# Kernel optimization log

Measured on AMD Instinct MI355X. Metric: run time of the kernel, lower is better.

The kernel has to match this reference:

```python
import jax, jax.numpy as jnp
import numpy as np

DIM = 1024
HDS = 16
HEAD_DIM = DIM // HDS
ISC = True


def setup_inputs() -> dict:
    key = jax.random.key(0)
    k = jax.random.split(key, 5)
    x = jax.random.normal(k[0], (4, 2048, DIM), dtype=jnp.float32)
    # Linear(dim, 3*dim): weight [3*dim, dim] (torch layout), bias [3*dim]
    scale = 1.0 / np.sqrt(DIM)
    w_qkv = jax.random.uniform(k[1], (3 * DIM, DIM), jnp.float32, -scale, scale)
    b_qkv = jax.random.uniform(k[2], (3 * DIM,), jnp.float32, -scale, scale)
    w_out = jax.random.uniform(k[3], (DIM, DIM), jnp.float32, -scale, scale)
    b_out = jax.random.uniform(k[4], (DIM,), jnp.float32, -scale, scale)
    return {"x": x, "w_qkv": w_qkv, "b_qkv": b_qkv, "w_out": w_out, "b_out": b_out}


def reference(x, w_qkv, b_qkv, w_out, b_out):
    b, s, dim = x.shape
    # QKV projection: x @ w_qkv.T + b_qkv -> split into q, k, v
    qkv = jnp.einsum('bsd,ed->bse', x, w_qkv) + b_qkv
    q, k, v = jnp.split(qkv, 3, axis=-1)
    # [b, s, dim] -> [b, h, s, hd]
    def to_heads(t):
        return t.reshape(b, s, HDS, HEAD_DIM).transpose(0, 2, 1, 3)
    q, k, v = to_heads(q), to_heads(k), to_heads(v)
    att = jnp.einsum('bhqd,bhkd->bhqk', q, k) * (HEAD_DIM ** -0.5)
    if ISC:
        mask = jnp.triu(jnp.ones((s, s), dtype=bool), k=1)  # True above diagonal
        att = jnp.where(mask[None, None], -jnp.inf, att)
    att = jax.nn.softmax(att, axis=-1)
    # dropout is identity in eval mode
    out = jnp.einsum('bhqk,bhkd->bhqd', att, v)
    out = out.transpose(0, 2, 1, 3).reshape(b, s, dim)
    out = jnp.einsum('bsd,ed->bse', out, w_out) + b_out
    return out
```

## Files before the change

kernel.cpp:

```cpp
#include <hip/hip_runtime.h>
#include <stdint.h>

typedef __bf16 bf16x8 __attribute__((ext_vector_type(8)));
typedef short s16x8 __attribute__((ext_vector_type(8)));
typedef short s16x4 __attribute__((ext_vector_type(4)));
typedef float f32x4 __attribute__((ext_vector_type(4)));
typedef unsigned short u16;

#define K_DIM 1024

static __device__ __forceinline__ u16 f2bf(float f) {
    uint32_t x = __float_as_uint(f);
    x += 0x7fffu + ((x >> 16) & 1u);
    return (u16)(x >> 16);
}

static __device__ __forceinline__ f32x4 mfma16(s16x8 a, s16x8 b, f32x4 c) {
    return __builtin_amdgcn_mfma_f32_16x16x32_bf16(
        __builtin_bit_cast(bf16x8, a), __builtin_bit_cast(bf16x8, b), c, 0, 0, 0);
}

static __device__ __forceinline__ void gload16(const u16* g, u16* l) {
    __builtin_amdgcn_global_load_lds(
        (const __attribute__((address_space(1))) void*)g,
        (__attribute__((address_space(3))) void*)l,
        16, 0, 0);
}

static __device__ __forceinline__ uint32_t cvt_pk_bf16(float lo, float hi) {
    uint32_t r;
    asm("v_cvt_pk_bf16_f32 %0, %1, %2" : "=v"(r) : "v"(lo), "v"(hi));
    return r;
}

static __device__ __forceinline__ float fexp2(float x) {
#if __has_builtin(__builtin_amdgcn_exp2f)
    return __builtin_amdgcn_exp2f(x);
#else
    return __expf(x * 0.69314718056f);
#endif
}

__global__ void cvt_f2bf(const float* __restrict__ in, u16* __restrict__ out, int n4) {
    int stride = gridDim.x * blockDim.x;
    for (int i = blockIdx.x * blockDim.x + threadIdx.x; i < n4; i += stride) {
        float4 f = ((const float4*)in)[i];
        ushort4 o;
        o.x = f2bf(f.x); o.y = f2bf(f.y); o.z = f2bf(f.z); o.w = f2bf(f.w);
        ((ushort4*)out)[i] = o;
    }
}

__global__ __launch_bounds__(256) void gemm_qkv(
    const u16* __restrict__ A, const u16* __restrict__ B,
    const float* __restrict__ bias,
    u16* __restrict__ qo, u16* __restrict__ ko, u16* __restrict__ vto)
{
    __shared__ u16 smem[32768];
    u16* ct = smem;
    const int tid = threadIdx.x;
    const int w = tid >> 6, l = tid & 63;
    const int lr = l & 15, lc = l >> 4;

    const int f = blockIdx.y * 64 + blockIdx.x;
    const int c = f & 7, j = f >> 3;
    const int m0 = (c * 8 + (j & 7)) * 128;
    const int n0 = (j >> 3) * 128;
    const int wm = (w >> 1) * 64, wn = (w & 1) * 64;

    const int srow = w * 8 + (l >> 3);
    const int scol = ((l & 7) ^ (l >> 3)) * 8;
    const u16* gA = A + (size_t)(m0 + srow) * K_DIM + scol;
    const u16* gB = B + (size_t)(n0 + srow) * K_DIM + scol;

    f32x4 acc[4][4] = {};

    auto stage = [&](int k0, int buf) {
        u16* base = smem + buf * 16384;
        #pragma unroll
        for (int g = 0; g < 4; ++g) {
            gload16(gA + (size_t)g * 32 * K_DIM + k0, base + (g * 32 + w * 8) * 64);
            gload16(gB + (size_t)g * 32 * K_DIM + k0, base + 8192 + (g * 32 + w * 8) * 64);
        }
    };

    stage(0, 0);
    int cur = 0;

    for (int k0 = 0; k0 < K_DIM; k0 += 64) {
        __syncthreads();
        if (k0 + 64 < K_DIM) stage(k0 + 64, cur ^ 1);
        const u16* As = smem + cur * 16384;
        const u16* Bs = As + 8192;
        #pragma unroll
        for (int kk = 0; kk < 2; ++kk) {
            s16x8 a[4], b[4];
            #pragma unroll
            for (int i = 0; i < 4; ++i) {
                const int row = wm + i * 16 + lr;
                a[i] = *(const s16x8*)&As[row * 64 + ((kk * 32 + lc * 8) ^ ((row & 7) * 8))];
            }
            #pragma unroll
            for (int jn = 0; jn < 4; ++jn) {
                const int row = wn + jn * 16 + lr;
                b[jn] = *(const s16x8*)&Bs[row * 64 + ((kk * 32 + lc * 8) ^ ((row & 7) * 8))];
            }
            #pragma unroll
            for (int i = 0; i < 4; ++i)
                #pragma unroll
                for (int jn = 0; jn < 4; ++jn)
                    acc[i][jn] = mfma16(a[i], b[jn], acc[i][jn]);
        }
        cur ^= 1;
    }

    const int sec = n0 >> 10;
    const int bb = m0 >> 11, s0 = m0 & 2047;

    if (sec < 2) {
        #pragma unroll
        for (int jn = 0; jn < 4; ++jn) {
            const int n = n0 + wn + jn * 16 + lr;
            const float bv = bias[n];
            const int h = (n & 1023) >> 6, d = n & 63;
            #pragma unroll
            for (int i = 0; i < 4; ++i) {
                #pragma unroll
                for (int r = 0; r < 4; ++r) {
                    const int m = m0 + wm + i * 16 + lc * 4 + r;
                    const int s = m & 2047;
                    float v = acc[i][jn][r] + bv;
                    if (sec == 0)
                        qo[((size_t)((bb * 16 + h) * 2048 + s)) * 64 + d] = f2bf(v * 0.18033688f);
                    else
                        ko[((size_t)((bb * 16 + h) * 2048 + s)) * 64 + d] = f2bf(v);
                }
            }
        }
    } else {
        __syncthreads();
        #pragma unroll
        for (int jj = 0; jj < 4; ++jj) {
            const int nl = (wn >> 6) * 16 + lr;
            const float bv = bias[n0 + wn + jj * 16 + lr];
            #pragma unroll
            for (int i = 0; i < 4; ++i) {
                const int mloc = wm + i * 16 + lc * 4;
                uint2 pk;
                pk.x = cvt_pk_bf16(acc[i][jj][0] + bv, acc[i][jj][1] + bv);
                pk.y = cvt_pk_bf16(acc[i][jj][2] + bv, acc[i][jj][3] + bv);
                *(s16x4*)&ct[nl * 136 + mloc] = __builtin_bit_cast(s16x4, pk);
            }
            __syncthreads();
            #pragma unroll
            for (int rep = 0; rep < 2; ++rep) {
                const int col = tid >> 3;
                const int seg = (tid & 7) + rep * 8;
                const int nn = n0 + (col >> 4) * 64 + jj * 16 + (col & 15);
                const int h = (nn & 1023) >> 6, d = nn & 63;
                const int mo = seg * 8;
                s16x8 v = *(const s16x8*)&ct[col * 136 + mo];
                *(s16x8*)&vto[((size_t)((bb * 16 + h) * 64 + d)) * 2048 + s0 + mo] = v;
            }
            __syncthreads();
        }
    }
}

__global__ __launch_bounds__(256, 2) void attn_fwd(
    const u16* __restrict__ q, const u16* __restrict__ k,
    const u16* __restrict__ vt, u16* __restrict__ ao)
{
    __shared__ u16 kt[2][8 * 512];
    __shared__ u16 vtl[2][8 * 512];
    __shared__ u16 plds[4 * 32 * 72];
    const int w = threadIdx.x >> 6, l = threadIdx.x & 63;
    const int lr = l & 15, lc = l >> 4;
    const int bh = blockIdx.x;
    const int cp = blockIdx.y;
    const u16* qp = q + (size_t)bh * 2048 * 64;
    const u16* kp = k + (size_t)bh * 2048 * 64;
    const u16* vp = vt + (size_t)bh * 64 * 2048;
    u16* pl = &plds[w * 2304];
    const int bb = bh >> 4, h = bh & 15;

    for (int pass = 0; pass < 2; ++pass) {
        const int C = pass ? (15 - cp) : cp;
        const int q0 = C * 128 + w * 32;
        const int nb = 2 * C + 2;
        const int diag = 2 * C + (w >> 1);

        s16x8 aQ[2][2];
        #pragma unroll
        for (int i = 0; i < 2; ++i)
            #pragma unroll
            for (int kk = 0; kk < 2; ++kk)
                aQ[i][kk] = *(const s16x8*)&qp[(q0 + i * 16 + lr) * 64 + kk * 32 + lc * 8];

        f32x4 O[2][4] = {};
        f32x4 lsv[2] = {};

        auto stage = [&](int t, int buf) {
            const int c0 = t * 64;
            if (w < 2) {
                #pragma unroll
                for (int gi = 0; gi < 4; ++gi) {
                    const int g = w * 4 + gi;
                    const int jx = g >> 1, kk = g & 1;
                    gload16(kp + (c0 + jx * 16 + lr) * 64 + kk * 32 + lc * 8,
                            &kt[buf][g * 512]);
                }
            } else {
                #pragma unroll
                for (int gi = 0; gi < 4; ++gi) {
                    const int g = (w - 2) * 4 + gi;
                    const int jd = g >> 1, kk = g & 1;
                    gload16(vp + (jd * 16 + lr) * 2048 + c0 + kk * 32 + lc * 8,
                            &vtl[buf][g * 512]);
                }
            }
        };

        __syncthreads();
        stage(0, 0);
        int cur = 0;

        for (int t = 0; t < nb; ++t) {
            __syncthreads();
            if (t + 1 < nb) stage(t + 1, cur ^ 1);

            if (t <= diag) {
                const int c0 = t * 64;
                f32x4 s[2][4] = {};
                __builtin_amdgcn_s_setprio(1);
                #pragma unroll
                for (int jx = 0; jx < 4; ++jx) {
                    s16x8 k0 = *(const s16x8*)&kt[cur][(jx * 2 + 0) * 512 + l * 8];
                    s16x8 k1 = *(const s16x8*)&kt[cur][(jx * 2 + 1) * 512 + l * 8];
                    s[0][jx] = mfma16(k0, aQ[0][0], s[0][jx]);
                    s[0][jx] = mfma16(k1, aQ[0][1], s[0][jx]);
                    s[1][jx] = mfma16(k0, aQ[1][0], s[1][jx]);
                    s[1][jx] = mfma16(k1, aQ[1][1], s[1][jx]);
                }
                __builtin_amdgcn_s_setprio(0);
                if (t == diag) {
                    #pragma unroll
                    for (int i = 0; i < 2; ++i) {
                        const int qrow = q0 + i * 16 + lr;
                        #pragma unroll
                        for (int jx = 0; jx < 4; ++jx) {
                            const int kvb = c0 + jx * 16 + lc * 4;
                            #pragma unroll
                            for (int r = 0; r < 4; ++r)
                                if (kvb + r > qrow) s[i][jx][r] = -1e30f;
                        }
                    }
                }
                #pragma unroll
                for (int i = 0; i < 2; ++i) {
                    #pragma unroll
                    for (int jx = 0; jx < 4; ++jx)
                        #pragma unroll
                        for (int r = 0; r < 4; ++r)
                            s[i][jx][r] = fexp2(s[i][jx][r]);
                    lsv[i] += (s[i][0] + s[i][1]) + (s[i][2] + s[i][3]);
                    #pragma unroll
                    for (int jx = 0; jx < 4; ++jx) {
                        uint2 pk;
                        pk.x = cvt_pk_bf16(s[i][jx][0], s[i][jx][1]);
                        pk.y = cvt_pk_bf16(s[i][jx][2], s[i][jx][3]);
                        *(s16x4*)&pl[(i * 16 + lr) * 72 + jx * 16 + lc * 4] =
                            __builtin_bit_cast(s16x4, pk);
                    }
                }
                s16x8 aP[2][2];
                #pragma unroll
                for (int i = 0; i < 2; ++i)
                    #pragma unroll
                    for (int kk = 0; kk < 2; ++kk)
                        aP[i][kk] = *(const s16x8*)&pl[(i * 16 + lr) * 72 + kk * 32 + lc * 8];
                __builtin_amdgcn_s_setprio(1);
                #pragma unroll
                for (int jd = 0; jd < 4; ++jd) {
                    s16x8 v0 = *(const s16x8*)&vtl[cur][(jd * 2 + 0) * 512 + l * 8];
                    s16x8 v1 = *(const s16x8*)&vtl[cur][(jd * 2 + 1) * 512 + l * 8];
                    O[0][jd] = mfma16(aP[0][0], v0, O[0][jd]);
                    O[0][jd] = mfma16(aP[0][1], v1, O[0][jd]);
                    O[1][jd] = mfma16(aP[1][0], v0, O[1][jd]);
                    O[1][jd] = mfma16(aP[1][1], v1, O[1][jd]);
                }
                __builtin_amdgcn_s_setprio(0);
            }
            cur ^= 1;
        }

        float lsr[2];
        #pragma unroll
        for (int i = 0; i < 2; ++i) {
            float t2 = (lsv[i][0] + lsv[i][1]) + (lsv[i][2] + lsv[i][3]);
            t2 += __shfl_xor(t2, 16);
            t2 += __shfl_xor(t2, 32);
            lsr[i] = 1.0f / t2;
        }
        float inv[2][4];
        #pragma unroll
        for (int i = 0; i < 2; ++i)
            #pragma unroll
            for (int r = 0; r < 4; ++r)
                inv[i][r] = __shfl(lsr[i], lc * 4 + r);

        #pragma unroll
        for (int i = 0; i < 2; ++i)
            #pragma unroll
            for (int jd = 0; jd < 4; ++jd)
                #pragma unroll
                for (int r = 0; r < 4; ++r) {
                    const int srow = q0 + i * 16 + lc * 4 + r;
                    ao[((size_t)(bb * 2048 + srow)) * 1024 + h * 64 + jd * 16 + lr] =
                        f2bf(O[i][jd][r] * inv[i][r]);
                }
    }
}

__global__ __launch_bounds__(256) void gemm_out(
    const u16* __restrict__ A, const u16* __restrict__ B,
    const float* __restrict__ bias, float* __restrict__ out)
{
    __shared__ u16 smem[32768];
    const int tid = threadIdx.x;
    const int w = tid >> 6, l = tid & 63;
    const int lr = l & 15, lc = l >> 4;

    const int f = blockIdx.y * 64 + blockIdx.x;
    const int c = f & 7, j = f >> 3;
    const int m0 = (c * 8 + (j & 7)) * 128;
    const int n0 = (j >> 3) * 128;
    const int wm = (w >> 1) * 64, wn = (w & 1) * 64;

    const int srow = w * 8 + (l >> 3);
    const int scol = ((l & 7) ^ (l >> 3)) * 8;
    const u16* gA = A + (size_t)(m0 + srow) * K_DIM + scol;
    const u16* gB = B + (size_t)(n0 + srow) * K_DIM + scol;

    f32x4 acc[4][4] = {};

    auto stage = [&](int k0, int buf) {
        u16* base = smem + buf * 16384;
        #pragma unroll
        for (int g = 0; g < 4; ++g) {
            gload16(gA + (size_t)g * 32 * K_DIM + k0, base + (g * 32 + w * 8) * 64);
            gload16(gB + (size_t)g * 32 * K_DIM + k0, base + 8192 + (g * 32 + w * 8) * 64);
        }
    };

    stage(0, 0);
    int cur = 0;

    for (int k0 = 0; k0 < K_DIM; k0 += 64) {
        __syncthreads();
        if (k0 + 64 < K_DIM) stage(k0 + 64, cur ^ 1);
        const u16* As = smem + cur * 16384;
        const u16* Bs = As + 8192;
        #pragma unroll
        for (int kk = 0; kk < 2; ++kk) {
            s16x8 a[4], b[4];
            #pragma unroll
            for (int i = 0; i < 4; ++i) {
                const int row = wm + i * 16 + lr;
                a[i] = *(const s16x8*)&As[row * 64 + ((kk * 32 + lc * 8) ^ ((row & 7) * 8))];
            }
            #pragma unroll
            for (int jn = 0; jn < 4; ++jn) {
                const int row = wn + jn * 16 + lr;
                b[jn] = *(const s16x8*)&Bs[row * 64 + ((kk * 32 + lc * 8) ^ ((row & 7) * 8))];
            }
            #pragma unroll
            for (int i = 0; i < 4; ++i)
                #pragma unroll
                for (int jn = 0; jn < 4; ++jn)
                    acc[i][jn] = mfma16(a[i], b[jn], acc[i][jn]);
        }
        cur ^= 1;
    }

    #pragma unroll
    for (int jn = 0; jn < 4; ++jn) {
        const int n = n0 + wn + jn * 16 + lr;
        const float bv = bias[n];
        #pragma unroll
        for (int i = 0; i < 4; ++i) {
            #pragma unroll
            for (int r = 0; r < 4; ++r) {
                const int m = m0 + wm + i * 16 + lc * 4 + r;
                out[(size_t)m * 1024 + n] = acc[i][jn][r] + bv;
            }
        }
    }
}

extern "C" void kernel_launch(void* const* d_in, const int* in_sizes, int n_in,
                              void* d_out, int out_size, void* d_ws, size_t ws_size,
                              hipStream_t stream) {
    const float* x     = (const float*)d_in[0];
    const float* w_qkv = (const float*)d_in[1];
    const float* b_qkv = (const float*)d_in[2];
    const float* w_out = (const float*)d_in[3];
    const float* b_out = (const float*)d_in[4];
    float* out = (float*)d_out;

    char* ws = (char*)d_ws;
    u16* xb   = (u16*)(ws);
    u16* wqb  = (u16*)(ws + 16777216);
    u16* wob  = (u16*)(ws + 23068672);
    u16* qws  = (u16*)(ws + 25165824);
    u16* kws  = (u16*)(ws + 41943040);
    u16* vtws = (u16*)(ws + 58720256);
    u16* attn = (u16*)(ws + 75497472);

    cvt_f2bf<<<dim3(2048), 256, 0, stream>>>(x,     xb,  8388608 / 4);
    cvt_f2bf<<<dim3(2048), 256, 0, stream>>>(w_qkv, wqb, 3145728 / 4);
    cvt_f2bf<<<dim3(1024), 256, 0, stream>>>(w_out, wob, 1048576 / 4);

    gemm_qkv<<<dim3(64, 24), 256, 0, stream>>>(xb, wqb, b_qkv, qws, kws, vtws);
    attn_fwd<<<dim3(64, 8), 256, 0, stream>>>(qws, kws, vtws, attn);
    gemm_out<<<dim3(64, 8), 256, 0, stream>>>(attn, wob, b_out, out);
}
```

Before: 135.7 us.

## Merge conversion kernels, split attention into one chunk per block, raise occupancy

Combines the three fp32-to-bf16 conversion launches into a single kernel to save launch overhead. The attention kernel no longer pairs chunks C and 15-C in one block. It launches 16 chunks per head, heaviest first, so the scheduler balances the causal workload. Occupancy is hinted at 3 blocks per SM, and the V fragments are loaded before masking and softmax to hide LDS latency. The cost is more blocks, each reloading Q and restarting the pipeline, plus register pressure from the tighter launch bound.

```diff
diff --git a/kernel.cpp b/kernel.cpp
--- a/kernel.cpp
+++ b/kernel.cpp
@@ -41,13 +41,29 @@
 #endif
 }
 
-__global__ void cvt_f2bf(const float* __restrict__ in, u16* __restrict__ out, int n4) {
-    int stride = gridDim.x * blockDim.x;
-    for (int i = blockIdx.x * blockDim.x + threadIdx.x; i < n4; i += stride) {
-        float4 f = ((const float4*)in)[i];
+__global__ void cvt_all(const float* __restrict__ x, const float* __restrict__ wq,
+                        const float* __restrict__ wo,
+                        u16* __restrict__ xb, u16* __restrict__ wqb,
+                        u16* __restrict__ wob) {
+    const int stride = gridDim.x * blockDim.x;
+    const int tid = blockIdx.x * blockDim.x + threadIdx.x;
+    for (int i = tid; i < 2097152; i += stride) {
+        float4 f = ((const float4*)x)[i];
         ushort4 o;
         o.x = f2bf(f.x); o.y = f2bf(f.y); o.z = f2bf(f.z); o.w = f2bf(f.w);
-        ((ushort4*)out)[i] = o;
+        ((ushort4*)xb)[i] = o;
+    }
+    for (int i = tid; i < 786432; i += stride) {
+        float4 f = ((const float4*)wq)[i];
+        ushort4 o;
+        o.x = f2bf(f.x); o.y = f2bf(f.y); o.z = f2bf(f.z); o.w = f2bf(f.w);
+        ((ushort4*)wqb)[i] = o;
+    }
+    for (int i = tid; i < 262144; i += stride) {
+        float4 f = ((const float4*)wo)[i];
+        ushort4 o;
+        o.x = f2bf(f.x); o.y = f2bf(f.y); o.z = f2bf(f.z); o.w = f2bf(f.w);
+        ((ushort4*)wob)[i] = o;
     }
 }
 
@@ -167,7 +183,7 @@
     }
 }
 
-__global__ __launch_bounds__(256, 2) void attn_fwd(
+__global__ __launch_bounds__(256, 3) void attn_fwd(
     const u16* __restrict__ q, const u16* __restrict__ k,
     const u16* __restrict__ vt, u16* __restrict__ ao)
 {
@@ -177,149 +193,149 @@
     const int w = threadIdx.x >> 6, l = threadIdx.x & 63;
     const int lr = l & 15, lc = l >> 4;
     const int bh = blockIdx.x;
-    const int cp = blockIdx.y;
+    const int C = 15 - blockIdx.y;
     const u16* qp = q + (size_t)bh * 2048 * 64;
     const u16* kp = k + (size_t)bh * 2048 * 64;
     const u16* vp = vt + (size_t)bh * 64 * 2048;
     u16* pl = &plds[w * 2304];
     const int bb = bh >> 4, h = bh & 15;
 
-    for (int pass = 0; pass < 2; ++pass) {
-        const int C = pass ? (15 - cp) : cp;
-        const int q0 = C * 128 + w * 32;
-        const int nb = 2 * C + 2;
-        const int diag = 2 * C + (w >> 1);
-
-        s16x8 aQ[2][2];
-        #pragma unroll
-        for (int i = 0; i < 2; ++i)
-            #pragma unroll
-            for (int kk = 0; kk < 2; ++kk)
-                aQ[i][kk] = *(const s16x8*)&qp[(q0 + i * 16 + lr) * 64 + kk * 32 + lc * 8];
-
-        f32x4 O[2][4] = {};
-        f32x4 lsv[2] = {};
-
-        auto stage = [&](int t, int buf) {
+    const int q0 = C * 128 + w * 32;
+    const int nb = 2 * C + 2;
+    const int diag = 2 * C + (w >> 1);
+
+    s16x8 aQ[2][2];
+    #pragma unroll
+    for (int i = 0; i < 2; ++i)
+        #pragma unroll
+        for (int kk = 0; kk < 2; ++kk)
+            aQ[i][kk] = *(const s16x8*)&qp[(q0 + i * 16 + lr) * 64 + kk * 32 + lc * 8];
+
+    f32x4 O[2][4] = {};
+    f32x4 lsv[2] = {};
+
+    auto stage = [&](int t, int buf) {
+        const int c0 = t * 64;
+        if (w < 2) {
+            #pragma unroll
+            for (int gi = 0; gi < 4; ++gi) {
+                const int g = w * 4 + gi;
+                const int jx = g >> 1, kk = g & 1;
+                gload16(kp + (c0 + jx * 16 + lr) * 64 + kk * 32 + lc * 8,
+                        &kt[buf][g * 512]);
+            }
+        } else {
+            #pragma unroll
+            for (int gi = 0; gi < 4; ++gi) {
+                const int g = (w - 2) * 4 + gi;
+                const int jd = g >> 1, kk = g & 1;
+                gload16(vp + (jd * 16 + lr) * 2048 + c0 + kk * 32 + lc * 8,
+                        &vtl[buf][g * 512]);
+            }
+        }
+    };
+
+    stage(0, 0);
+    int cur = 0;
+
+    for (int t = 0; t < nb; ++t) {
+        __syncthreads();
+        if (t + 1 < nb) stage(t + 1, cur ^ 1);
+
+        if (t <= diag) {
             const int c0 = t * 64;
-            if (w < 2) {
-                #pragma unroll
-                for (int gi = 0; gi < 4; ++gi) {
-                    const int g = w * 4 + gi;
-                    const int jx = g >> 1, kk = g & 1;
-                    gload16(kp + (c0 + jx * 16 + lr) * 64 + kk * 32 + lc * 8,
-                            &kt[buf][g * 512]);
-                }
-            } else {
-                #pragma unroll
-                for (int gi = 0; gi < 4; ++gi) {
-                    const int g = (w - 2) * 4 + gi;
-                    const int jd = g >> 1, kk = g & 1;
-                    gload16(vp + (jd * 16 + lr) * 2048 + c0 + kk * 32 + lc * 8,
-                            &vtl[buf][g * 512]);
-                }
-            }
-        };
-
-        __syncthreads();
-        stage(0, 0);
-        int cur = 0;
-
-        for (int t = 0; t < nb; ++t) {
-            __syncthreads();
-            if (t + 1 < nb) stage(t + 1, cur ^ 1);
-
-            if (t <= diag) {
-                const int c0 = t * 64;
-                f32x4 s[2][4] = {};
-                __builtin_amdgcn_s_setprio(1);
-                #pragma unroll
-                for (int jx = 0; jx < 4; ++jx) {
-                    s16x8 k0 = *(const s16x8*)&kt[cur][(jx * 2 + 0) * 512 + l * 8];
-                    s16x8 k1 = *(const s16x8*)&kt[cur][(jx * 2 + 1) * 512 + l * 8];
-                    s[0][jx] = mfma16(k0, aQ[0][0], s[0][jx]);
-                    s[0][jx] = mfma16(k1, aQ[0][1], s[0][jx]);
-                    s[1][jx] = mfma16(k0, aQ[1][0], s[1][jx]);
-                    s[1][jx] = mfma16(k1, aQ[1][1], s[1][jx]);
-                }
-                __builtin_amdgcn_s_setprio(0);
-                if (t == diag) {
+            f32x4 s[2][4] = {};
+            __builtin_amdgcn_s_setprio(1);
+            #pragma unroll
+            for (int jx = 0; jx < 4; ++jx) {
+                s16x8 k0 = *(const s16x8*)&kt[cur][(jx * 2 + 0) * 512 + l * 8];
+                s16x8 k1 = *(const s16x8*)&kt[cur][(jx * 2 + 1) * 512 + l * 8];
+                s[0][jx] = mfma16(k0, aQ[0][0], s[0][jx]);
+                s[0][jx] = mfma16(k1, aQ[0][1], s[0][jx]);
+                s[1][jx] = mfma16(k0, aQ[1][0], s[1][jx]);
+                s[1][jx] = mfma16(k1, aQ[1][1], s[1][jx]);
+            }
+            __builtin_amdgcn_s_setprio(0);
+            s16x8 vf[4][2];
+            #pragma unroll
+            for (int jd = 0; jd < 4; ++jd)
+                #pragma unroll
+                for (int kk = 0; kk < 2; ++kk)
+                    vf[jd][kk] = *(const s16x8*)&vtl[cur][(jd * 2 + kk) * 512 + l * 8];
+            if (t == diag) {
+                #pragma unroll
+                for (int i = 0; i < 2; ++i) {
+                    const int qrow = q0 + i * 16 + lr;
                     #pragma unroll
-                    for (int i = 0; i < 2; ++i) {
-                        const int qrow = q0 + i * 16 + lr;
+                    for (int jx = 0; jx < 4; ++jx) {
+                        const int kvb = c0 + jx * 16 + lc * 4;
                         #pragma unroll
-                        for (int jx = 0; jx < 4; ++jx) {
-                            const int kvb = c0 + jx * 16 + lc * 4;
-                            #pragma unroll
-                            for (int r = 0; r < 4; ++r)
-                                if (kvb + r > qrow) s[i][jx][r] = -1e30f;
-                        }
+                        for (int r = 0; r < 4; ++r)
+                            if (kvb + r > qrow) s[i][jx][r] = -1e30f;
                     }
                 }
-                #pragma unroll
-                for (int i = 0; i < 2; ++i) {
+            }
+            #pragma unroll
+            for (int i = 0; i < 2; ++i) {
+                #pragma unroll
+                for (int jx = 0; jx < 4; ++jx)
                     #pragma unroll
-                    for (int jx = 0; jx < 4; ++jx)
-                        #pragma unroll
-                        for (int r = 0; r < 4; ++r)
-                            s[i][jx][r] = fexp2(s[i][jx][r]);
-                    lsv[i] += (s[i][0] + s[i][1]) + (s[i][2] + s[i][3]);
-                    #pragma unroll
-                    for (int jx = 0; jx < 4; ++jx) {
-                        uint2 pk;
-                        pk.x = cvt_pk_bf16(s[i][jx][0], s[i][jx][1]);
-                        pk.y = cvt_pk_bf16(s[i][jx][2], s[i][jx][3]);
-                        *(s16x4*)&pl[(i * 16 + lr) * 72 + jx * 16 + lc * 4] =
-                            __builtin_bit_cast(s16x4, pk);
-                    }
+                    for (int r = 0; r < 4; ++r)
+                        s[i][jx][r] = fexp2(s[i][jx][r]);
+                lsv[i] += (s[i][0] + s[i][1]) + (s[i][2] + s[i][3]);
+                #pragma unroll
+                for (int jx = 0; jx < 4; ++jx) {
+                    uint2 pk;
+                    pk.x = cvt_pk_bf16(s[i][jx][0], s[i][jx][1]);
+                    pk.y = cvt_pk_bf16(s[i][jx][2], s[i][jx][3]);
+                    *(s16x4*)&pl[(i * 16 + lr) * 72 + jx * 16 + lc * 4] =
+                        __builtin_bit_cast(s16x4, pk);
                 }
-                s16x8 aP[2][2];
-                #pragma unroll
-                for (int i = 0; i < 2; ++i)
-                    #pragma unroll
-                    for (int kk = 0; kk < 2; ++kk)
-                        aP[i][kk] = *(const s16x8*)&pl[(i * 16 + lr) * 72 + kk * 32 + lc * 8];
-                __builtin_amdgcn_s_setprio(1);
-                #pragma unroll
-                for (int jd = 0; jd < 4; ++jd) {
-                    s16x8 v0 = *(const s16x8*)&vtl[cur][(jd * 2 + 0) * 512 + l * 8];
-                    s16x8 v1 = *(const s16x8*)&vtl[cur][(jd * 2 + 1) * 512 + l * 8];
-                    O[0][jd] = mfma16(aP[0][0], v0, O[0][jd]);
-                    O[0][jd] = mfma16(aP[0][1], v1, O[0][jd]);
-                    O[1][jd] = mfma16(aP[1][0], v0, O[1][jd]);
-                    O[1][jd] = mfma16(aP[1][1], v1, O[1][jd]);
-                }
-                __builtin_amdgcn_s_setprio(0);
-            }
-            cur ^= 1;
-        }
-
-        float lsr[2];
-        #pragma unroll
-        for (int i = 0; i < 2; ++i) {
-            float t2 = (lsv[i][0] + lsv[i][1]) + (lsv[i][2] + lsv[i][3]);
-            t2 += __shfl_xor(t2, 16);
-            t2 += __shfl_xor(t2, 32);
-            lsr[i] = 1.0f / t2;
-        }
-        float inv[2][4];
-        #pragma unroll
-        for (int i = 0; i < 2; ++i)
-            #pragma unroll
-            for (int r = 0; r < 4; ++r)
-                inv[i][r] = __shfl(lsr[i], lc * 4 + r);
-
-        #pragma unroll
-        for (int i = 0; i < 2; ++i)
-            #pragma unroll
-            for (int jd = 0; jd < 4; ++jd)
-                #pragma unroll
-                for (int r = 0; r < 4; ++r) {
-                    const int srow = q0 + i * 16 + lc * 4 + r;
-                    ao[((size_t)(bb * 2048 + srow)) * 1024 + h * 64 + jd * 16 + lr] =
-                        f2bf(O[i][jd][r] * inv[i][r]);
-                }
-    }
+            }
+            s16x8 aP[2][2];
+            #pragma unroll
+            for (int i = 0; i < 2; ++i)
+                #pragma unroll
+                for (int kk = 0; kk < 2; ++kk)
+                    aP[i][kk] = *(const s16x8*)&pl[(i * 16 + lr) * 72 + kk * 32 + lc * 8];
+            __builtin_amdgcn_s_setprio(1);
+            #pragma unroll
+            for (int jd = 0; jd < 4; ++jd) {
+                O[0][jd] = mfma16(aP[0][0], vf[jd][0], O[0][jd]);
+                O[0][jd] = mfma16(aP[0][1], vf[jd][1], O[0][jd]);
+                O[1][jd] = mfma16(aP[1][0], vf[jd][0], O[1][jd]);
+                O[1][jd] = mfma16(aP[1][1], vf[jd][1], O[1][jd]);
+            }
+            __builtin_amdgcn_s_setprio(0);
+        }
+        cur ^= 1;
+    }
+
+    float lsr[2];
+    #pragma unroll
+    for (int i = 0; i < 2; ++i) {
+        float t2 = (lsv[i][0] + lsv[i][1]) + (lsv[i][2] + lsv[i][3]);
+        t2 += __shfl_xor(t2, 16);
+        t2 += __shfl_xor(t2, 32);
+        lsr[i] = 1.0f / t2;
+    }
+    float inv[2][4];
+    #pragma unroll
+    for (int i = 0; i < 2; ++i)
+        #pragma unroll
+        for (int r = 0; r < 4; ++r)
+            inv[i][r] = __shfl(lsr[i], lc * 4 + r);
+
+    #pragma unroll
+    for (int i = 0; i < 2; ++i)
+        #pragma unroll
+        for (int jd = 0; jd < 4; ++jd)
+            #pragma unroll
+            for (int r = 0; r < 4; ++r) {
+                const int srow = q0 + i * 16 + lc * 4 + r;
+                ao[((size_t)(bb * 2048 + srow)) * 1024 + h * 64 + jd * 16 + lr] =
+                    f2bf(O[i][jd][r] * inv[i][r]);
+            }
 }
 
 __global__ __launch_bounds__(256) void gemm_out(
@@ -417,11 +433,9 @@
     u16* vtws = (u16*)(ws + 58720256);
     u16* attn = (u16*)(ws + 75497472);
 
-    cvt_f2bf<<<dim3(2048), 256, 0, stream>>>(x,     xb,  8388608 / 4);
-    cvt_f2bf<<<dim3(2048), 256, 0, stream>>>(w_qkv, wqb, 3145728 / 4);
-    cvt_f2bf<<<dim3(1024), 256, 0, stream>>>(w_out, wob, 1048576 / 4);
+    cvt_all<<<dim3(2048), 256, 0, stream>>>(x, w_qkv, w_out, xb, wqb, wob);
 
     gemm_qkv<<<dim3(64, 24), 256, 0, stream>>>(xb, wqb, b_qkv, qws, kws, vtws);
-    attn_fwd<<<dim3(64, 8), 256, 0, stream>>>(qws, kws, vtws, attn);
+    attn_fwd<<<dim3(64, 16), 256, 0, stream>>>(qws, kws, vtws, attn);
     gemm_out<<<dim3(64, 8), 256, 0, stream>>>(attn, wob, b_out, out);
 }
```

Result: no change. 135.1 us (-0.4%).
